# Kernel tuning notes

Measured on AMD Instinct MI355X. Metric: run time of the kernel, lower is better.

The kernel has to match this reference:

```python
import jax, jax.numpy as jnp
import numpy as np

K = 512
H = 8

def setup_inputs() -> dict:
    key = jax.random.key(0)
    ks = jax.random.split(key, 6)
    b, t, k = 4, 2048, K
    scale = 1.0 / np.sqrt(k)
    return {
        "x": jax.random.normal(ks[0], (b, t, k), dtype=jnp.float32),
        "Wq": jax.random.normal(ks[1], (k, k), dtype=jnp.float32) * scale,
        "Wk": jax.random.normal(ks[2], (k, k), dtype=jnp.float32) * scale,
        "Wv": jax.random.normal(ks[3], (k, k), dtype=jnp.float32) * scale,
        "Wo": jax.random.normal(ks[4], (k, k), dtype=jnp.float32) * scale,
        "bo": jax.random.normal(ks[5], (k,), dtype=jnp.float32) * 0.01,
    }

def reference(x, Wq, Wk, Wv, Wo, bo):
    b, t, k = x.shape
    h = H
    s = k // h
    # nn.Linear: y = x @ W.T ; weights stored [out, in]
    q = (x @ Wq.T).reshape(b, t, h, s)
    kk = (x @ Wk.T).reshape(b, t, h, s)
    v = (x @ Wv.T).reshape(b, t, h, s)
    # scores: note original divides by sqrt(k) (full model dim), not sqrt(s)
    dot = jnp.einsum("bqhs,bkhs->bhqk", q, kk) / jnp.sqrt(jnp.float32(k))
    attn = jax.nn.softmax(dot, axis=-1)
    out = jnp.einsum("bhqk,bkhs->bqhs", attn, v).reshape(b, t, k)
    return out @ Wo.T + bo
```

## Files before the change

kernel.cpp:

```cpp
#include <hip/hip_runtime.h>

typedef _Float16 f16;
typedef _Float16 f16x8 __attribute__((ext_vector_type(8)));
typedef _Float16 f16x4 __attribute__((ext_vector_type(4)));
typedef float    f32x4 __attribute__((ext_vector_type(4)));
typedef __fp16   fp16x2 __attribute__((ext_vector_type(2)));

#define MFMA(a,b,c) __builtin_amdgcn_mfma_f32_16x16x32_f16((a),(b),(c),0,0,0)

#if __has_builtin(__builtin_amdgcn_exp2f)
#define EXP2(x) __builtin_amdgcn_exp2f(x)
#else
#define EXP2(x) exp2f(x)
#endif

__device__ __forceinline__ void gl_lds16(const void* g, void* l) {
  __builtin_amdgcn_global_load_lds(
      (__attribute__((address_space(1))) void*)(void*)(g),
      (__attribute__((address_space(3))) void*)(l),
      16, 0, 0);
}

__device__ __forceinline__ int SWZ(int row) {
  return ((row & 3) | ((row >> 1) & 4)) << 4;
}

__global__ __launch_bounds__(256) void k_convert(
    const float* __restrict__ x, const float* __restrict__ Wq,
    const float* __restrict__ Wk, const float* __restrict__ Wv,
    const float* __restrict__ Wo,
    f16* __restrict__ x_h, f16* __restrict__ wqkv_h, f16* __restrict__ wo_h) {
  const int XQ    = (8192 * 512) / 4;
  const int WQKVQ = (1536 * 512) / 4;
  const int WOQ   = (512 * 512) / 4;
  const int total = XQ + WQKVQ + WOQ;
  for (int q = blockIdx.x * blockDim.x + threadIdx.x; q < total;
       q += gridDim.x * blockDim.x) {
    const float* src;
    f16* dst;
    if (q < XQ) {
      src = x + q * 4;
      dst = x_h + q * 4;
    } else if (q < XQ + WQKVQ) {
      int j  = q - XQ;
      int r  = j >> 7;
      int c0 = (j & 127) * 4;
      const float* w = (r < 512) ? Wq : (r < 1024) ? Wk : Wv;
      src = w + (r & 511) * 512 + c0;
      dst = wqkv_h + j * 4;
    } else {
      int j = q - XQ - WQKVQ;
      src = Wo + j * 4;
      dst = wo_h + j * 4;
    }
    float4 v = *(const float4*)src;
    f16x4 o = {(f16)v.x, (f16)v.y, (f16)v.z, (f16)v.w};
    *(f16x4*)dst = o;
  }
}

__device__ __forceinline__ void gemm_core(const f16* __restrict__ A,
                                          const f16* __restrict__ B,
                                          int bm, int bn, f32x4 (&acc)[4][4],
                                          char* smem) {
  f16* As = (f16*)smem;
  f16* Bs = (f16*)(smem + 32768);
  const int tid  = threadIdx.x;
  const int lane = tid & 63;
  const int w    = tid >> 6;
  const int wr   = (w >> 1) & 1, wc = w & 1;
  const int r0   = tid >> 3;
  const int cb   = (tid & 7) << 4;

  auto stage = [&](int buf, int kt) {
#pragma unroll
    for (int inst = 0; inst < 4; ++inst) {
      const int row  = inst * 32 + r0;
      const int csrc = cb ^ ((row & 7) << 4);
      gl_lds16(A + (bm + row) * 512 + kt + (csrc >> 1),
               (char*)As + buf * 16384 + inst * 4096 + w * 1024);
      gl_lds16(B + (bn + row) * 512 + kt + (csrc >> 1),
               (char*)Bs + buf * 16384 + inst * 4096 + w * 1024);
    }
  };

  stage(0, 0);
#pragma unroll
  for (int t = 0; t < 8; ++t) {
    const int cur = t & 1;
    asm volatile("s_waitcnt vmcnt(0)" ::: "memory");
    __builtin_amdgcn_s_barrier();
    __builtin_amdgcn_sched_barrier(0);
    if (t < 7) stage(cur ^ 1, (t + 1) * 64);
    f16x8 af[4][2], bf[4][2];
#pragma unroll
    for (int i = 0; i < 4; ++i) {
      const int ra = wr * 64 + i * 16 + (lane & 15);
      const int rb = wc * 64 + i * 16 + (lane & 15);
#pragma unroll
      for (int ks = 0; ks < 2; ++ks) {
        const int cc = ks * 64 + ((lane >> 4) << 4);
        af[i][ks] = *(const f16x8*)((const char*)As + cur * 16384 + ra * 128 + (cc ^ ((ra & 7) << 4)));
        bf[i][ks] = *(const f16x8*)((const char*)Bs + cur * 16384 + rb * 128 + (cc ^ ((rb & 7) << 4)));
      }
    }
    __builtin_amdgcn_s_setprio(1);
#pragma unroll
    for (int i = 0; i < 4; ++i)
#pragma unroll
      for (int j = 0; j < 4; ++j) {
        acc[i][j] = MFMA(af[i][0], bf[j][0], acc[i][j]);
        acc[i][j] = MFMA(af[i][1], bf[j][1], acc[i][j]);
      }
    __builtin_amdgcn_s_setprio(0);
  }
}

__global__ __launch_bounds__(256) void k_gemm_qkv(
    const f16* __restrict__ A, const f16* __restrict__ B,
    f16* __restrict__ q_h, f16* __restrict__ k_h, f16* __restrict__ vt_h) {
  __shared__ char smem[65536];
  const int bm = blockIdx.x * 128;
  const int bn = blockIdx.y * 128;
  const bool isV = (bn >= 1024);

  f32x4 acc[4][4] = {};
  if (isV) gemm_core(B, A, bn, bm, acc, smem);
  else     gemm_core(A, B, bm, bn, acc, smem);

  const int tid  = threadIdx.x;
  const int lane = tid & 63;
  const int w    = tid >> 6;
  const int wr   = (w >> 1) & 1, wc = w & 1;
  const float qscale = (bn < 512) ? 0.044194173824159216f * 1.4426950408889634f : 1.0f;

  __syncthreads();
  f16* T = (f16*)smem;
#pragma unroll
  for (int i = 0; i < 4; ++i) {
    const int rr = wr * 64 + i * 16 + ((lane >> 4) << 2);
#pragma unroll
    for (int j = 0; j < 4; ++j) {
      const int cc = wc * 64 + j * 16 + (lane & 15);
#pragma unroll
      for (int r = 0; r < 4; ++r)
        T[(rr + r) * 136 + cc] = (f16)(acc[i][j][r] * qscale);
    }
  }
  __syncthreads();

  f16* dst_qk = (bn < 512) ? q_h : k_h;
#pragma unroll
  for (int k = 0; k < 8; ++k) {
    const int idx  = k * 256 + tid;
    const int row  = idx >> 4;
    const int col8 = (idx & 15) * 8;
    const f16x8 v = *(const f16x8*)(T + row * 136 + col8);
    if (!isV) {
      const int m = bm + row, b = m >> 11, t = m & 2047;
      const int nn = (bn + col8) & 511, h = nn >> 6, s = nn & 63;
      *(f16x8*)(dst_qk + ((size_t)((b * 8 + h) * 2048 + t)) * 64 + s) = v;
    } else {
      const int nn = (bn - 1024) + row, h = nn >> 6, s = nn & 63;
      const int m = bm + col8, b = m >> 11, t = m & 2047;
      *(f16x8*)(vt_h + ((size_t)((b * 8 + h) * 64 + s)) * 2048 + t) = v;
    }
  }
}

__global__ __launch_bounds__(512, 2) void k_attn(
    const f16* __restrict__ q_h, const f16* __restrict__ k_h,
    const f16* __restrict__ vt_h, f16* __restrict__ a_h) {
  __shared__ char smem[65536];

  const int tid  = threadIdx.x;
  const int lane = tid & 63;
  const int w    = tid >> 6;
  const int g    = w >> 2;
  const int wg   = w & 3;

  int id = blockIdx.x;
  id = (id & 7) * 32 + (id >> 3);
  const int qt = (id & 7) * 256;
  const int bh = id >> 3;

  const f16* qb = q_h + (size_t)bh * 2048 * 64;
  const f16* kb = k_h + (size_t)bh * 2048 * 64;
  const f16* vb = vt_h + (size_t)bh * 64 * 2048;

  auto KsP = [&](int grp, int buf) { return smem + grp * 32768 + buf * 16384; };
  auto VsP = [&](int grp, int buf) { return smem + grp * 32768 + buf * 16384 + 8192; };

  const int m  = lane & 15;
  const int hi = lane >> 4;

  f16x8 qf[4][2];
#pragma unroll
  for (int i = 0; i < 4; ++i) {
    const int qrow = qt + wg * 64 + i * 16 + m;
#pragma unroll
    for (int ks = 0; ks < 2; ++ks)
      qf[i][ks] = *(const f16x8*)(qb + qrow * 64 + ks * 32 + hi * 8);
  }

  f32x4 oacc[4][4] = {};
  f32x4 lrun[4]    = {};

  const int gt  = tid & 255;
  const int r0  = gt >> 3;
  const int cbb = (tid & 7) << 4;

  const f16 one = (f16)1.0f;
  const f16x8 ones = {one, one, one, one, one, one, one, one};

  auto stage = [&](int buf, int t) {
    const int ktv = g * 1024 + t * 64;
#pragma unroll
    for (int inst = 0; inst < 2; ++inst) {
      const int row  = inst * 32 + r0;
      const int csrc = cbb ^ SWZ(row);
      gl_lds16(kb + (ktv + row) * 64 + (csrc >> 1),
               KsP(g, buf) + inst * 4096 + wg * 1024);
      gl_lds16(vb + row * 2048 + ktv + (csrc >> 1),
               VsP(g, buf) + inst * 4096 + wg * 1024);
    }
  };

  auto pack4 = [](float a, float b, float c, float d) -> unsigned long long {
    union { fp16x2 h2[2]; unsigned long long u; } t;
    t.h2[0] = __builtin_amdgcn_cvt_pkrtz(a, b);
    t.h2[1] = __builtin_amdgcn_cvt_pkrtz(c, d);
    return t.u;
  };

  auto tile = [&](const char* ksb, const char* vsb) {
    f16x8 kf[4][2];
#pragma unroll
    for (int n = 0; n < 4; ++n) {
      const int row = ((n >> 1) << 5) + ((m >> 2) << 3) + ((n & 1) << 2) + (m & 3);
      const int sw  = SWZ(row);
#pragma unroll
      for (int ks = 0; ks < 2; ++ks) {
        const int c = (ks * 64 + (hi << 4)) ^ sw;
        kf[n][ks] = *(const f16x8*)(ksb + row * 128 + c);
      }
    }
    f32x4 sf[4][4];
    __builtin_amdgcn_s_setprio(1);
#pragma unroll
    for (int i = 0; i < 4; ++i)
#pragma unroll
      for (int n = 0; n < 4; ++n) {
        f32x4 s = {0.f, 0.f, 0.f, 0.f};
        s = MFMA(kf[n][0], qf[i][0], s);
        s = MFMA(kf[n][1], qf[i][1], s);
        sf[i][n] = s;
      }
    __builtin_amdgcn_s_setprio(0);
    f16x8 pa[4][2];
#pragma unroll
    for (int i = 0; i < 4; ++i)
#pragma unroll
      for (int ks = 0; ks < 2; ++ks) {
        union { unsigned long long u[2]; f16x8 v; } u;
        u.u[0] = pack4(EXP2(sf[i][2 * ks][0]), EXP2(sf[i][2 * ks][1]),
                       EXP2(sf[i][2 * ks][2]), EXP2(sf[i][2 * ks][3]));
        u.u[1] = pack4(EXP2(sf[i][2 * ks + 1][0]), EXP2(sf[i][2 * ks + 1][1]),
                       EXP2(sf[i][2 * ks + 1][2]), EXP2(sf[i][2 * ks + 1][3]));
        pa[i][ks] = u.v;
      }
    __builtin_amdgcn_s_setprio(1);
#pragma unroll
    for (int i = 0; i < 4; ++i) {
      lrun[i] = MFMA(pa[i][0], ones, lrun[i]);
      lrun[i] = MFMA(pa[i][1], ones, lrun[i]);
    }
#pragma unroll
    for (int n = 0; n < 4; ++n) {
      const int row = n * 16 + m;
      const int sw  = SWZ(row);
      const f16x8 vf0 = *(const f16x8*)(vsb + row * 128 + ((hi << 4) ^ sw));
      const f16x8 vf1 = *(const f16x8*)(vsb + row * 128 + ((64 + (hi << 4)) ^ sw));
#pragma unroll
      for (int i = 0; i < 4; ++i) {
        oacc[i][n] = MFMA(pa[i][0], vf0, oacc[i][n]);
        oacc[i][n] = MFMA(pa[i][1], vf1, oacc[i][n]);
      }
    }
    __builtin_amdgcn_s_setprio(0);
  };

  stage(0, 0);
  for (int j = 0; j < 16; ++j) {
    const int cur = j & 1;
    asm volatile("s_waitcnt vmcnt(0)" ::: "memory");
    __builtin_amdgcn_s_barrier();
    __builtin_amdgcn_sched_barrier(0);
    if (j < 15) stage(cur ^ 1, j + 1);
    tile(KsP(g, cur), VsP(g, cur));
  }

  __syncthreads();
  float* Ol = (float*)smem;
  float* l1 = (float*)(smem + 34816);

  const int b2 = bh >> 3, h2 = bh & 7;
#pragma unroll
  for (int p = 0; p < 2; ++p) {
    if (g == 1 && (wg >> 1) == p) {
#pragma unroll
      for (int i = 0; i < 4; ++i)
#pragma unroll
        for (int r = 0; r < 4; ++r) {
          const int ql = (wg * 64 + i * 16 + hi * 4 + r) & 127;
#pragma unroll
          for (int n = 0; n < 4; ++n)
            Ol[ql * 68 + n * 16 + m] = oacc[i][n][r];
          if (m == 0) l1[ql] = lrun[i][r];
        }
    }
    __syncthreads();
    if (g == 0 && (wg >> 1) == p) {
#pragma unroll
      for (int i = 0; i < 4; ++i)
#pragma unroll
        for (int r = 0; r < 4; ++r) {
          const int qg = wg * 64 + i * 16 + hi * 4 + r;
          const int ql = qg & 127;
          const float rl = 1.0f / (lrun[i][r] + l1[ql]);
          const int qrow = qt + qg;
#pragma unroll
          for (int n = 0; n < 4; ++n) {
            const int s = n * 16 + m;
            const float o = oacc[i][n][r] + Ol[ql * 68 + s];
            a_h[(size_t)(b2 * 2048 + qrow) * 512 + h2 * 64 + s] = (f16)(o * rl);
          }
        }
    }
    __syncthreads();
  }
}

__global__ __launch_bounds__(256) void k_gemm_out(
    const f16* __restrict__ A, const f16* __restrict__ B,
    const float* __restrict__ bo, float* __restrict__ out) {
  __shared__ char smem[65536];
  const int bm = blockIdx.x * 128;
  const int bn = blockIdx.y * 128;
  f32x4 acc[4][4] = {};
  gemm_core(A, B, bm, bn, acc, smem);

  const int tid  = threadIdx.x;
  const int lane = tid & 63;
  const int w    = tid >> 6;
  const int wr   = (w >> 1) & 1, wc = w & 1;
#pragma unroll
  for (int i = 0; i < 4; ++i) {
    const int m0 = bm + wr * 64 + i * 16 + ((lane >> 4) << 2);
#pragma unroll
    for (int j = 0; j < 4; ++j) {
      const int n = bn + wc * 64 + j * 16 + (lane & 15);
      const float bias = bo[n];
#pragma unroll
      for (int r = 0; r < 4; ++r)
        out[(size_t)(m0 + r) * 512 + n] = acc[i][j][r] + bias;
    }
  }
}

extern "C" void kernel_launch(void* const* d_in, const int* in_sizes, int n_in,
                              void* d_out, int out_size, void* d_ws, size_t ws_size,
                              hipStream_t stream) {
  const float* x  = (const float*)d_in[0];
  const float* Wq = (const float*)d_in[1];
  const float* Wk = (const float*)d_in[2];
  const float* Wv = (const float*)d_in[3];
  const float* Wo = (const float*)d_in[4];
  const float* bo = (const float*)d_in[5];
  float* out = (float*)d_out;

  char* ws = (char*)d_ws;
  f16* x_h    = (f16*)(ws);
  f16* wqkv_h = (f16*)(ws + 8388608);
  f16* wo_h   = (f16*)(ws + 9961472);
  f16* q_h    = (f16*)(ws + 10485760);
  f16* k_h    = (f16*)(ws + 18874368);
  f16* vt_h   = (f16*)(ws + 27262976);
  f16* a_h    = (f16*)(ws + 35651584);
  (void)ws_size; (void)in_sizes; (void)n_in; (void)out_size;

  k_convert<<<2048, 256, 0, stream>>>(x, Wq, Wk, Wv, Wo, x_h, wqkv_h, wo_h);
  k_gemm_qkv<<<dim3(64, 12), 256, 0, stream>>>(x_h, wqkv_h, q_h, k_h, vt_h);
  k_attn<<<256, 512, 0, stream>>>(q_h, k_h, vt_h, a_h);
  k_gemm_out<<<dim3(64, 4), 256, 0, stream>>>(a_h, wo_h, bo, out);
}
```

Before: 80.43 us.

## Software-pipeline attention loop: overlap QK/exp of next tile with PV of previous

Splits the per-tile attention body into QK, exp, and PV phases and software-pipelines them so the QK MFMAs and exp of tile t interleave with the PV MFMAs of tile t-1. Buffering moves from double to triple, growing LDS per block from 64KB to 96KB, and two sets of P fragments are kept live in registers. The intent is to hide transcendental/exp latency behind matrix work; the cost is higher register pressure and LDS use, which could reduce occupancy with two 512-thread blocks per CU.

```diff
diff --git a/kernel.cpp b/kernel.cpp
--- a/kernel.cpp
+++ b/kernel.cpp
@@ -171,7 +171,7 @@
 __global__ __launch_bounds__(512, 2) void k_attn(
     const f16* __restrict__ q_h, const f16* __restrict__ k_h,
     const f16* __restrict__ vt_h, f16* __restrict__ a_h) {
-  __shared__ char smem[65536];
+  __shared__ char smem[98304];
 
   const int tid  = threadIdx.x;
   const int lane = tid & 63;
@@ -188,8 +188,8 @@
   const f16* kb = k_h + (size_t)bh * 2048 * 64;
   const f16* vb = vt_h + (size_t)bh * 64 * 2048;
 
-  auto KsP = [&](int grp, int buf) { return smem + grp * 32768 + buf * 16384; };
-  auto VsP = [&](int grp, int buf) { return smem + grp * 32768 + buf * 16384 + 8192; };
+  auto KsP = [&](int grp, int buf) { return smem + grp * 49152 + buf * 16384; };
+  auto VsP = [&](int grp, int buf) { return smem + grp * 49152 + buf * 16384 + 8192; };
 
   const int m  = lane & 15;
   const int hi = lane >> 4;
@@ -233,7 +233,9 @@
     return t.u;
   };
 
-  auto tile = [&](const char* ksb, const char* vsb) {
+  f32x4 sf[4][4];
+
+  auto do_qk = [&](const char* ksb) {
     f16x8 kf[4][2];
 #pragma unroll
     for (int n = 0; n < 4; ++n) {
@@ -245,7 +247,6 @@
         kf[n][ks] = *(const f16x8*)(ksb + row * 128 + c);
       }
     }
-    f32x4 sf[4][4];
     __builtin_amdgcn_s_setprio(1);
 #pragma unroll
     for (int i = 0; i < 4; ++i)
@@ -257,7 +258,9 @@
         sf[i][n] = s;
       }
     __builtin_amdgcn_s_setprio(0);
-    f16x8 pa[4][2];
+  };
+
+  auto do_exp = [&](f16x8 (&pa)[4][2]) {
 #pragma unroll
     for (int i = 0; i < 4; ++i)
 #pragma unroll
@@ -269,6 +272,9 @@
                        EXP2(sf[i][2 * ks + 1][2]), EXP2(sf[i][2 * ks + 1][3]));
         pa[i][ks] = u.v;
       }
+  };
+
+  auto do_pv = [&](const char* vsb, f16x8 (&pa)[4][2]) {
     __builtin_amdgcn_s_setprio(1);
 #pragma unroll
     for (int i = 0; i < 4; ++i) {
@@ -290,14 +296,32 @@
     __builtin_amdgcn_s_setprio(0);
   };
 
-  stage(0, 0);
-  for (int j = 0; j < 16; ++j) {
-    const int cur = j & 1;
+  f16x8 paA[4][2], paB[4][2];
+
+  auto step = [&](int t, f16x8 (&paOld)[4][2], f16x8 (&paNew)[4][2],
+                  bool doQK, bool doStage) {
     asm volatile("s_waitcnt vmcnt(0)" ::: "memory");
     __builtin_amdgcn_s_barrier();
     __builtin_amdgcn_sched_barrier(0);
-    if (j < 15) stage(cur ^ 1, j + 1);
-    tile(KsP(g, cur), VsP(g, cur));
+    const int cur = t % 3, prev = (t + 2) % 3, nxt = (t + 1) % 3;
+    if (doStage) stage(nxt, t + 1);
+    if (doQK) do_qk(KsP(g, cur));
+    do_pv(VsP(g, prev), paOld);
+    if (doQK) do_exp(paNew);
+  };
+
+  stage(0, 0);
+  asm volatile("s_waitcnt vmcnt(0)" ::: "memory");
+  __builtin_amdgcn_s_barrier();
+  __builtin_amdgcn_sched_barrier(0);
+  stage(1, 1);
+  do_qk(KsP(g, 0));
+  do_exp(paA);
+
+  for (int tt = 0; tt < 8; ++tt) {
+    const int t1 = 2 * tt + 1, t2 = 2 * tt + 2;
+    step(t1, paA, paB, true, t1 + 1 < 16);
+    step(t2, paB, paA, t2 < 16, t2 + 1 < 16);
   }
 
   __syncthreads();
```

Measured after the change: 81.39 us. No clear change (+1.2%).
